# Kernel tuning notes

Measured on AMD Instinct MI355X. Metric: run time of the kernel, lower is better.

## Reference

```python
import jax, jax.numpy as jnp
import numpy as np

N_NODES = 50000
N_RAND_EDGES = 800000
IN_DIM = 128
HEADS = 4
OUT_FEATS = 32
NEG_SLOPE = 0.2  # DGL GATConv default


def setup_inputs() -> dict:
    key = jax.random.key(0)
    k1, k2, k3, k4, k5, k6 = jax.random.split(key, 6)
    h = jax.random.normal(k1, (N_NODES, IN_DIM), dtype=jnp.float32)
    fc_w = jax.random.normal(k2, (HEADS * OUT_FEATS, IN_DIM), dtype=jnp.float32) * 0.1
    attn_l = jax.random.normal(k3, (HEADS, OUT_FEATS), dtype=jnp.float32) * 0.1
    attn_r = jax.random.normal(k4, (HEADS, OUT_FEATS), dtype=jnp.float32) * 0.1
    src_r = jax.random.randint(k5, (N_RAND_EDGES,), 0, N_NODES, dtype=jnp.int32)
    dst_r = jax.random.randint(k6, (N_RAND_EDGES,), 0, N_NODES, dtype=jnp.int32)
    loops = jnp.arange(N_NODES, dtype=jnp.int32)
    src = jnp.concatenate([src_r, loops])  # self-loops ensure in_degree >= 1
    dst = jnp.concatenate([dst_r, loops])
    return {"h": h, "fc_w": fc_w, "attn_l": attn_l, "attn_r": attn_r,
            "src": src, "dst": dst}


def reference(h, fc_w, attn_l, attn_r, src, dst):
    N = h.shape[0]
    # linear projection, reshape to [N, H, D]
    hf = (h @ fc_w.T).reshape(N, HEADS, OUT_FEATS)
    # per-node attention halves: el = <hf, a_l>, er = <hf, a_r>  -> [N, H]
    el = jnp.einsum('nhd,hd->nh', hf, attn_l)
    er = jnp.einsum('nhd,hd->nh', hf, attn_r)
    # edge scores: u_add_v + leaky_relu  -> [E, H]
    e = jax.nn.leaky_relu(el[src] + er[dst], negative_slope=NEG_SLOPE)
    # segment softmax over incoming edges of each dst node
    m = jax.ops.segment_max(e, dst, num_segments=N)
    ex = jnp.exp(e - m[dst])
    s = jax.ops.segment_sum(ex, dst, num_segments=N)
    a = ex / s[dst]  # [E, H]
    # weighted neighbor aggregation: u_mul_e then segment sum
    msg = hf[src] * a[:, :, None]  # [E, H, D]
    out = jax.ops.segment_sum(msg, dst, num_segments=N)  # [N, H, D]
    return out.reshape(N, HEADS * OUT_FEATS), a[:, :, None]
```

## Files before the change

### kernel.cpp

```cpp
#include <hip/hip_runtime.h>
#include <hip/hip_bf16.h>

#define NEG 0.2f
#define BSTRIDE 8192

typedef float vf4 __attribute__((ext_vector_type(4)));
typedef int   vi4 __attribute__((ext_vector_type(4)));
typedef short bf8 __attribute__((ext_vector_type(8)));
typedef float f32x4 __attribute__((ext_vector_type(4)));

__device__ __forceinline__ float leaky(float x){ return x > 0.f ? x : NEG*x; }
__device__ __forceinline__ float sel4(float4 q, int head){
  float lo = (head & 1) ? q.y : q.x;
  float hi = (head & 1) ? q.w : q.z;
  return (head & 2) ? hi : lo;
}
__device__ __forceinline__ float b2f_lo(unsigned u){ return __uint_as_float(u << 16); }
__device__ __forceinline__ float b2f_hi(unsigned u){ return __uint_as_float(u & 0xffff0000u); }
__device__ __forceinline__ float b2f(unsigned short u){ return __uint_as_float((unsigned)u << 16); }
__device__ __forceinline__ unsigned short f2b(float f){
  __hip_bfloat16 b = __float2bfloat16(f);
  return *(unsigned short*)&b;
}
__device__ __forceinline__ vi4 ntload_i4(const int* p){
  return __builtin_nontemporal_load((const vi4*)p);
}
__device__ __forceinline__ void ntstore_f4(float* p, float a, float b, float c, float d){
  vf4 v; v.x = a; v.y = b; v.z = c; v.w = d;
  __builtin_nontemporal_store(v, (vf4*)p);
}

__global__ __launch_bounds__(256) void k_wconv(const float* __restrict__ fcw,
    unsigned short* __restrict__ fcw16, int* __restrict__ bcur) {
  const int tid = threadIdx.x;
  if (blockIdx.x == 0) bcur[tid] = tid * BSTRIDE;
  const int i = (blockIdx.x*256 + tid) * 8;
  float4 w0 = *(const float4*)&fcw[i];
  float4 w1 = *(const float4*)&fcw[i + 4];
  unsigned short q[8];
  q[0]=f2b(w0.x); q[1]=f2b(w0.y); q[2]=f2b(w0.z); q[3]=f2b(w0.w);
  q[4]=f2b(w1.x); q[5]=f2b(w1.y); q[6]=f2b(w1.z); q[7]=f2b(w1.w);
  *(uint4*)&fcw16[i] = *(const uint4*)q;
}

__global__ __launch_bounds__(256) void k_proj(
    const float* __restrict__ h, const unsigned short* __restrict__ fcw16,
    const float* __restrict__ attn_l, const float* __restrict__ attn_r,
    unsigned short* __restrict__ hf16, float* __restrict__ el, float* __restrict__ er, int N)
{
  __shared__ __align__(16) unsigned short hs[4][16*128];

  const int tid = threadIdx.x;
  const int wave = tid >> 6, lane = tid & 63;
  const int r = lane & 15, khi = lane >> 4;
  const int nb0 = blockIdx.x*64 + wave*16;
  int gn_a = nb0 + r; if (gn_a >= N) gn_a = N-1;
  const float* hp = &h[(size_t)gn_a*128];

  bf8 afr[4];
  #pragma unroll
  for (int ks = 0; ks < 4; ++ks) {
    const float* p = hp + ks*32 + khi*8;
    float4 w0 = *(const float4*)p;
    float4 w1 = *(const float4*)(p + 4);
    bf8 a;
    a[0]=(short)f2b(w0.x); a[1]=(short)f2b(w0.y); a[2]=(short)f2b(w0.z); a[3]=(short)f2b(w0.w);
    a[4]=(short)f2b(w1.x); a[5]=(short)f2b(w1.y); a[6]=(short)f2b(w1.z); a[7]=(short)f2b(w1.w);
    afr[ks] = a;
  }

  f32x4 acc[8];
  #pragma unroll
  for (int ct = 0; ct < 8; ++ct) { acc[ct][0]=0.f; acc[ct][1]=0.f; acc[ct][2]=0.f; acc[ct][3]=0.f; }

  #pragma unroll
  for (int ct = 0; ct < 8; ++ct) {
    const int f = ct*16 + r;
    #pragma unroll
    for (int ks = 0; ks < 4; ++ks) {
      bf8 b = *(const bf8*)&fcw16[(size_t)f*128 + ks*32 + khi*8];
      acc[ct] = __builtin_amdgcn_mfma_f32_16x16x32_bf16(afr[ks], b, acc[ct], 0, 0, 0);
    }
  }

  unsigned short* hw = &hs[wave][0];
  #pragma unroll
  for (int ct = 0; ct < 8; ++ct) {
    const int ftile = ct*16 + r;
    #pragma unroll
    for (int j = 0; j < 4; ++j)
      hw[(khi*4 + j)*128 + ftile] = f2b(acc[ct][j]);
  }

  for (int i = lane; i < 16*16; i += 64) {
    int row = i >> 4, ch = i & 15;
    int gn = nb0 + row;
    if (gn < N)
      *(uint4*)&hf16[(size_t)gn*128 + ch*8] = *(const uint4*)&hw[row*128 + ch*8];
  }

  {
    const int row = lane >> 2, head = lane & 3;
    const int gn = nb0 + row;
    const unsigned short* hr = &hw[row*128 + head*32];
    const float* alp = &attn_l[head*32];
    const float* arp = &attn_r[head*32];
    float e_l = 0.f, e_r = 0.f;
    #pragma unroll
    for (int ff = 0; ff < 32; ++ff) {
      float hv = b2f(hr[ff]);
      e_l += hv * alp[ff];
      e_r += hv * arp[ff];
    }
    if (gn < N) {
      el[(size_t)gn*4 + head] = e_l;
      er[(size_t)gn*4 + head] = e_r;
    }
  }
}

#define TILE 4096
__global__ __launch_bounds__(1024) void k_bin(
    const int* __restrict__ src, const int* __restrict__ dst,
    int* __restrict__ bcur, unsigned int* __restrict__ staging, int E)
{
  __shared__ unsigned int lpack[TILE];
  __shared__ unsigned char lbkt[TILE];
  __shared__ unsigned short sidx[TILE];
  __shared__ int lhist[256], lbase[256], lcur[256], gbase[256];

  const int t = threadIdx.x;
  const int e0 = blockIdx.x * TILE;
  const int cnt = min(TILE, E - e0);

  if (t < 256) lhist[t] = 0;
  __syncthreads();

  for (int i = t; i < cnt; i += 1024) {
    int s = __builtin_nontemporal_load(&src[e0 + i]);
    int d = __builtin_nontemporal_load(&dst[e0 + i]);
    lpack[i] = ((unsigned)(d & 255) << 24) | (unsigned)s;
    int b = d >> 8;
    lbkt[i] = (unsigned char)b;
    atomicAdd(&lhist[b], 1);
  }
  __syncthreads();

  __shared__ int ltmp[256];
  if (t < 256) ltmp[t] = lhist[t];
  __syncthreads();
  for (int off = 1; off < 256; off <<= 1) {
    int x = 0;
    if (t < 256 && t >= off) x = ltmp[t - off];
    __syncthreads();
    if (t < 256) ltmp[t] += x;
    __syncthreads();
  }
  if (t < 256) { lbase[t] = ltmp[t] - lhist[t]; lcur[t] = ltmp[t] - lhist[t]; }
  __syncthreads();

  for (int i = t; i < cnt; i += 1024) {
    int p = atomicAdd(&lcur[lbkt[i]], 1);
    sidx[p] = (unsigned short)i;
  }
  if (t < 256) {
    int c = lhist[t];
    gbase[t] = c ? atomicAdd(&bcur[t], c) : 0;
  }
  __syncthreads();

  for (int p = t; p < cnt; p += 1024) {
    int j = sidx[p];
    int b = lbkt[j];
    staging[gbase[b] + (p - lbase[b])] = lpack[j];
  }
}

__global__ __launch_bounds__(1024) void k_debin(
    const unsigned int* __restrict__ staging, const int* __restrict__ bcur,
    int* __restrict__ esrc, int* __restrict__ offsets, int* __restrict__ degs, int N)
{
  __shared__ int lout[BSTRIDE];
  __shared__ int lhist[256], lexcl[256], lcur[256];

  const int t = threadIdx.x;
  const int b = blockIdx.x;
  const int n0 = b << 8;
  const int nb = min(256, N - n0);
  const int out_start = b * BSTRIDE;
  const int cnt = bcur[b] - out_start;

  if (t < 256) lhist[t] = 0;
  __syncthreads();

  for (int i = t; i < cnt; i += 1024)
    atomicAdd(&lhist[staging[out_start + i] >> 24], 1);
  __syncthreads();

  if (t < 256) lexcl[t] = lhist[t];
  __syncthreads();
  for (int off = 1; off < 256; off <<= 1) {
    int x = 0;
    if (t < 256 && t >= off) x = lexcl[t - off];
    __syncthreads();
    if (t < 256) lexcl[t] += x;
    __syncthreads();
  }
  if (t < 256) {
    int ex = lexcl[t] - lhist[t];
    lexcl[t] = ex;
    lcur[t]  = ex;
  }
  __syncthreads();

  for (int i = t; i < cnt; i += 1024) {
    unsigned int w = staging[out_start + i];
    int p = atomicAdd(&lcur[w >> 24], 1);
    lout[p] = (int)(w & 0x00FFFFFFu);
  }
  __syncthreads();
  for (int i = t; i < cnt; i += 1024)
    esrc[out_start + i] = lout[i];

  if (t < nb) {
    offsets[n0 + t] = out_start + lexcl[t];
    degs[n0 + t]    = lhist[t];
  }
}

__global__ __launch_bounds__(256) void k_aggr(
    const int* __restrict__ esrc, const int* __restrict__ offsets, const int* __restrict__ degs,
    const unsigned short* __restrict__ hf16, const float* __restrict__ el, const float* __restrict__ er,
    float* __restrict__ out, float* __restrict__ mr, int N)
{
  __shared__ float as[4][64][4];
  __shared__ int   es[4][64];
  const int wave = threadIdx.x >> 6, lane = threadIdx.x & 63;
  const int v = blockIdx.x*4 + wave;
  if (v >= N) return;
  const int start = offsets[v];
  const int deg   = degs[v];
  const float4 er4 = *(const float4*)&er[(size_t)v*4];

  const bool act = lane < deg;
  float4 x4 = make_float4(0.f, 0.f, 0.f, 0.f);
  int mys = 0;
  if (act) {
    mys = esrc[start + lane];
    float4 el4 = *(const float4*)&el[(size_t)mys*4];
    x4.x = __expf(leaky(el4.x + er4.x));
    x4.y = __expf(leaky(el4.y + er4.y));
    x4.z = __expf(leaky(el4.z + er4.z));
    x4.w = __expf(leaky(el4.w + er4.w));
  }
  float4 s4 = x4;
  for (int j = lane + 64; j < deg; j += 64) {
    int s = esrc[start + j];
    float4 el4 = *(const float4*)&el[(size_t)s*4];
    s4.x += __expf(leaky(el4.x + er4.x));
    s4.y += __expf(leaky(el4.y + er4.y));
    s4.z += __expf(leaky(el4.z + er4.z));
    s4.w += __expf(leaky(el4.w + er4.w));
  }
  #pragma unroll
  for (int mm = 32; mm; mm >>= 1) {
    s4.x += __shfl_xor(s4.x, mm);
    s4.y += __shfl_xor(s4.y, mm);
    s4.z += __shfl_xor(s4.z, mm);
    s4.w += __shfl_xor(s4.w, mm);
  }
  const float4 r4 = make_float4(1.f/s4.x, 1.f/s4.y, 1.f/s4.z, 1.f/s4.w);

  if (act) {
    float4 a4 = make_float4(x4.x*r4.x, x4.y*r4.y, x4.z*r4.z, x4.w*r4.w);
    *(float4*)&as[wave][lane][0] = a4;
    es[wave][lane] = mys;
  }
  if (lane == 0) *(float4*)&mr[(size_t)v*4] = r4;

  const int g = lane >> 3;
  const int l = lane & 7;
  const int head = l >> 1;
  float acc[16];
  #pragma unroll
  for (int k = 0; k < 16; ++k) acc[k] = 0.f;

  const int degL = deg < 64 ? deg : 64;
  {
    int je = g;
    int jec = je < degL ? je : 0;
    int sj = es[wave][jec];
    float a = je < degL ? as[wave][jec][head] : 0.f;
    const unsigned short* hp = &hf16[(size_t)sj*128 + 16*l];
    uint4 q0 = *(const uint4*)hp;
    uint4 q1 = *(const uint4*)(hp + 8);
    for (int j = 0; j < degL; j += 8) {
      int je2 = j + 8 + g;
      int jec2 = je2 < degL ? je2 : 0;
      int s2 = es[wave][jec2];
      float a2 = je2 < degL ? as[wave][jec2][head] : 0.f;
      const unsigned short* hp2 = &hf16[(size_t)s2*128 + 16*l];
      uint4 p0 = *(const uint4*)hp2;
      uint4 p1 = *(const uint4*)(hp2 + 8);
      acc[0]  += a*b2f_lo(q0.x); acc[1]  += a*b2f_hi(q0.x);
      acc[2]  += a*b2f_lo(q0.y); acc[3]  += a*b2f_hi(q0.y);
      acc[4]  += a*b2f_lo(q0.z); acc[5]  += a*b2f_hi(q0.z);
      acc[6]  += a*b2f_lo(q0.w); acc[7]  += a*b2f_hi(q0.w);
      acc[8]  += a*b2f_lo(q1.x); acc[9]  += a*b2f_hi(q1.x);
      acc[10] += a*b2f_lo(q1.y); acc[11] += a*b2f_hi(q1.y);
      acc[12] += a*b2f_lo(q1.z); acc[13] += a*b2f_hi(q1.z);
      acc[14] += a*b2f_lo(q1.w); acc[15] += a*b2f_hi(q1.w);
      q0 = p0; q1 = p1; a = a2;
    }
  }
  for (int j = 64; j < deg; j += 8) {
    const int je = j + g;
    const bool valid = je < deg;
    int s = esrc[start + (valid ? je : 0)];
    float rh = sel4(r4, head), erh = sel4(er4, head);
    float a = __expf(leaky(el[(size_t)s*4 + head] + erh)) * rh;
    if (!valid) a = 0.f;
    const unsigned short* hp = &hf16[(size_t)s*128 + 16*l];
    uint4 q0 = *(const uint4*)hp;
    uint4 q1 = *(const uint4*)(hp + 8);
    acc[0]  += a*b2f_lo(q0.x); acc[1]  += a*b2f_hi(q0.x);
    acc[2]  += a*b2f_lo(q0.y); acc[3]  += a*b2f_hi(q0.y);
    acc[4]  += a*b2f_lo(q0.z); acc[5]  += a*b2f_hi(q0.z);
    acc[6]  += a*b2f_lo(q0.w); acc[7]  += a*b2f_hi(q0.w);
    acc[8]  += a*b2f_lo(q1.x); acc[9]  += a*b2f_hi(q1.x);
    acc[10] += a*b2f_lo(q1.y); acc[11] += a*b2f_hi(q1.y);
    acc[12] += a*b2f_lo(q1.z); acc[13] += a*b2f_hi(q1.z);
    acc[14] += a*b2f_lo(q1.w); acc[15] += a*b2f_hi(q1.w);
  }

  #pragma unroll
  for (int k = 0; k < 16; ++k) {
    acc[k] += __shfl_xor(acc[k], 8);
    acc[k] += __shfl_xor(acc[k], 16);
    acc[k] += __shfl_xor(acc[k], 32);
  }
  if (g == 0) {
    float* op = &out[(size_t)v*128 + 16*l];
    ntstore_f4(op,      acc[0],  acc[1],  acc[2],  acc[3]);
    ntstore_f4(op + 4,  acc[4],  acc[5],  acc[6],  acc[7]);
    ntstore_f4(op + 8,  acc[8],  acc[9],  acc[10], acc[11]);
    ntstore_f4(op + 12, acc[12], acc[13], acc[14], acc[15]);
  }
}

__global__ void k_attn(const int* __restrict__ src, const int* __restrict__ dst,
                       const float* __restrict__ el, const float* __restrict__ er,
                       const float* __restrict__ mr, float* __restrict__ a_out, int E) {
  int e0 = (blockIdx.x*256 + threadIdx.x)*4;
  if (e0 + 3 < E) {
    vi4 sv = ntload_i4(&src[e0]);
    vi4 dv = ntload_i4(&dst[e0]);
    #pragma unroll
    for (int k = 0; k < 4; ++k) {
      int s = (k==0)?sv.x:(k==1)?sv.y:(k==2)?sv.z:sv.w;
      int d = (k==0)?dv.x:(k==1)?dv.y:(k==2)?dv.z:dv.w;
      float4 el4 = *(const float4*)&el[(size_t)s*4];
      float4 er4 = *(const float4*)&er[(size_t)d*4];
      float4 c4  = *(const float4*)&mr[(size_t)d*4];
      ntstore_f4(&a_out[(size_t)(e0+k)*4],
                 __expf(leaky(el4.x + er4.x)) * c4.x,
                 __expf(leaky(el4.y + er4.y)) * c4.y,
                 __expf(leaky(el4.z + er4.z)) * c4.z,
                 __expf(leaky(el4.w + er4.w)) * c4.w);
    }
  } else {
    for (int e = e0; e < E; ++e) {
      int s = src[e], d = dst[e];
      float4 el4 = *(const float4*)&el[(size_t)s*4];
      float4 er4 = *(const float4*)&er[(size_t)d*4];
      float4 c4  = *(const float4*)&mr[(size_t)d*4];
      ntstore_f4(&a_out[(size_t)e*4],
                 __expf(leaky(el4.x + er4.x)) * c4.x,
                 __expf(leaky(el4.y + er4.y)) * c4.y,
                 __expf(leaky(el4.z + er4.z)) * c4.z,
                 __expf(leaky(el4.w + er4.w)) * c4.w);
    }
  }
}

extern "C" void kernel_launch(void* const* d_in, const int* in_sizes, int n_in,
                              void* d_out, int out_size, void* d_ws, size_t ws_size,
                              hipStream_t stream) {
  const float* h      = (const float*)d_in[0];
  const float* fcw    = (const float*)d_in[1];
  const float* attn_l = (const float*)d_in[2];
  const float* attn_r = (const float*)d_in[3];
  const int*   src    = (const int*)d_in[4];
  const int*   dst    = (const int*)d_in[5];
  const int N = in_sizes[0] / 128;
  const int E = in_sizes[4];
  const int B = (N + 255) >> 8;

  float* out   = (float*)d_out;
  float* a_out = out + (size_t)N*128;

  char* w = (char*)d_ws;
  unsigned short* hf16 = (unsigned short*)w; w += (size_t)N*128*sizeof(unsigned short);
  unsigned short* fcw16 = (unsigned short*)w; w += (size_t)128*128*sizeof(unsigned short);
  float* el      = (float*)w; w += (size_t)N*4*sizeof(float);
  float* er      = (float*)w; w += (size_t)N*4*sizeof(float);
  float* mr      = (float*)w; w += (size_t)N*4*sizeof(float);
  int*   esrc    = (int*)w;   w += (size_t)256*BSTRIDE*sizeof(int);
  unsigned int* staging = (unsigned int*)w; w += (size_t)256*BSTRIDE*sizeof(unsigned int);
  int*   offsets = (int*)w;   w += (size_t)N*sizeof(int);
  int*   degs    = (int*)w;   w += (size_t)N*sizeof(int);
  int*   bcur    = (int*)w;   w += 256*sizeof(int);

  k_wconv<<<8, 256, 0, stream>>>(fcw, fcw16, bcur);

  k_proj<<<(N + 63)/64, 256, 0, stream>>>(h, fcw16, attn_l, attn_r, hf16, el, er, N);

  k_bin<<<(E + TILE - 1)/TILE, 1024, 0, stream>>>(src, dst, bcur, staging, E);
  k_debin<<<B, 1024, 0, stream>>>(staging, bcur, esrc, offsets, degs, N);

  k_aggr<<<(N + 3)/4, 256, 0, stream>>>(esrc, offsets, degs, hf16, el, er, out, mr, N);

  k_attn<<<(E/4 + 255)/256 + 1, 256, 0, stream>>>(src, dst, el, er, mr, a_out, E);
}
```

Baseline: 116.3 us.

## Fuse weight bf16 conversion into projection kernel with swizzled LDS weight tile

Removes the separate weight-conversion kernel. Each projection block now converts the fp32 weight matrix to bf16 into a 32KB XOR-swizzled LDS tile and reads MFMA B fragments from LDS rather than global memory. Each block now handles 128 nodes in two passes, which amortises the per-block conversion. This saves one kernel launch and the global re-reads of the weights, but every block redoes the conversion and the larger LDS footprint reduces occupancy.

```diff
diff --git a/kernel.cpp b/kernel.cpp
--- a/kernel.cpp
+++ b/kernel.cpp
@@ -30,91 +30,97 @@
   __builtin_nontemporal_store(v, (vf4*)p);
 }
 
-__global__ __launch_bounds__(256) void k_wconv(const float* __restrict__ fcw,
-    unsigned short* __restrict__ fcw16, int* __restrict__ bcur) {
+__global__ __launch_bounds__(256) void k_proj(
+    const float* __restrict__ h, const float* __restrict__ fcw,
+    const float* __restrict__ attn_l, const float* __restrict__ attn_r,
+    unsigned short* __restrict__ hf16, float* __restrict__ el, float* __restrict__ er,
+    int* __restrict__ bcur, int N)
+{
+  __shared__ __align__(16) unsigned short fcs[128*128];
+  __shared__ __align__(16) unsigned short hs[4][16*128];
+
   const int tid = threadIdx.x;
   if (blockIdx.x == 0) bcur[tid] = tid * BSTRIDE;
-  const int i = (blockIdx.x*256 + tid) * 8;
-  float4 w0 = *(const float4*)&fcw[i];
-  float4 w1 = *(const float4*)&fcw[i + 4];
-  unsigned short q[8];
-  q[0]=f2b(w0.x); q[1]=f2b(w0.y); q[2]=f2b(w0.z); q[3]=f2b(w0.w);
-  q[4]=f2b(w1.x); q[5]=f2b(w1.y); q[6]=f2b(w1.z); q[7]=f2b(w1.w);
-  *(uint4*)&fcw16[i] = *(const uint4*)q;
-}
-
-__global__ __launch_bounds__(256) void k_proj(
-    const float* __restrict__ h, const unsigned short* __restrict__ fcw16,
-    const float* __restrict__ attn_l, const float* __restrict__ attn_r,
-    unsigned short* __restrict__ hf16, float* __restrict__ el, float* __restrict__ er, int N)
-{
-  __shared__ __align__(16) unsigned short hs[4][16*128];
-
-  const int tid = threadIdx.x;
+
+  for (int i = tid; i < 128*16; i += 256) {
+    int f = i >> 4, ch = i & 15;
+    const float* p = &fcw[(size_t)f*128 + ch*8];
+    float4 w0 = *(const float4*)p;
+    float4 w1 = *(const float4*)(p + 4);
+    unsigned short* q = &fcs[f*128 + (ch ^ (f & 7))*8];
+    q[0]=f2b(w0.x); q[1]=f2b(w0.y); q[2]=f2b(w0.z); q[3]=f2b(w0.w);
+    q[4]=f2b(w1.x); q[5]=f2b(w1.y); q[6]=f2b(w1.z); q[7]=f2b(w1.w);
+  }
+  __syncthreads();
+
   const int wave = tid >> 6, lane = tid & 63;
   const int r = lane & 15, khi = lane >> 4;
-  const int nb0 = blockIdx.x*64 + wave*16;
-  int gn_a = nb0 + r; if (gn_a >= N) gn_a = N-1;
-  const float* hp = &h[(size_t)gn_a*128];
-
-  bf8 afr[4];
-  #pragma unroll
-  for (int ks = 0; ks < 4; ++ks) {
-    const float* p = hp + ks*32 + khi*8;
-    float4 w0 = *(const float4*)p;
-    float4 w1 = *(const float4*)(p + 4);
-    bf8 a;
-    a[0]=(short)f2b(w0.x); a[1]=(short)f2b(w0.y); a[2]=(short)f2b(w0.z); a[3]=(short)f2b(w0.w);
-    a[4]=(short)f2b(w1.x); a[5]=(short)f2b(w1.y); a[6]=(short)f2b(w1.z); a[7]=(short)f2b(w1.w);
-    afr[ks] = a;
-  }
-
-  f32x4 acc[8];
-  #pragma unroll
-  for (int ct = 0; ct < 8; ++ct) { acc[ct][0]=0.f; acc[ct][1]=0.f; acc[ct][2]=0.f; acc[ct][3]=0.f; }
-
-  #pragma unroll
-  for (int ct = 0; ct < 8; ++ct) {
-    const int f = ct*16 + r;
+
+  for (int nt = 0; nt < 2; ++nt) {
+    const int nb0 = blockIdx.x*128 + nt*64 + wave*16;
+    int gn_a = nb0 + r; if (gn_a >= N) gn_a = N-1;
+    const float* hp = &h[(size_t)gn_a*128];
+
+    bf8 afr[4];
     #pragma unroll
     for (int ks = 0; ks < 4; ++ks) {
-      bf8 b = *(const bf8*)&fcw16[(size_t)f*128 + ks*32 + khi*8];
-      acc[ct] = __builtin_amdgcn_mfma_f32_16x16x32_bf16(afr[ks], b, acc[ct], 0, 0, 0);
-    }
-  }
-
-  unsigned short* hw = &hs[wave][0];
-  #pragma unroll
-  for (int ct = 0; ct < 8; ++ct) {
-    const int ftile = ct*16 + r;
+      const float* p = hp + ks*32 + khi*8;
+      float4 w0 = *(const float4*)p;
+      float4 w1 = *(const float4*)(p + 4);
+      bf8 a;
+      a[0]=(short)f2b(w0.x); a[1]=(short)f2b(w0.y); a[2]=(short)f2b(w0.z); a[3]=(short)f2b(w0.w);
+      a[4]=(short)f2b(w1.x); a[5]=(short)f2b(w1.y); a[6]=(short)f2b(w1.z); a[7]=(short)f2b(w1.w);
+      afr[ks] = a;
+    }
+
+    f32x4 acc[8];
     #pragma unroll
-    for (int j = 0; j < 4; ++j)
-      hw[(khi*4 + j)*128 + ftile] = f2b(acc[ct][j]);
-  }
-
-  for (int i = lane; i < 16*16; i += 64) {
-    int row = i >> 4, ch = i & 15;
-    int gn = nb0 + row;
-    if (gn < N)
-      *(uint4*)&hf16[(size_t)gn*128 + ch*8] = *(const uint4*)&hw[row*128 + ch*8];
-  }
-
-  {
-    const int row = lane >> 2, head = lane & 3;
-    const int gn = nb0 + row;
-    const unsigned short* hr = &hw[row*128 + head*32];
-    const float* alp = &attn_l[head*32];
-    const float* arp = &attn_r[head*32];
-    float e_l = 0.f, e_r = 0.f;
+    for (int ct = 0; ct < 8; ++ct) { acc[ct][0]=0.f; acc[ct][1]=0.f; acc[ct][2]=0.f; acc[ct][3]=0.f; }
+
     #pragma unroll
-    for (int ff = 0; ff < 32; ++ff) {
-      float hv = b2f(hr[ff]);
-      e_l += hv * alp[ff];
-      e_r += hv * arp[ff];
-    }
-    if (gn < N) {
-      el[(size_t)gn*4 + head] = e_l;
-      er[(size_t)gn*4 + head] = e_r;
+    for (int ct = 0; ct < 8; ++ct) {
+      const int f = ct*16 + r;
+      #pragma unroll
+      for (int ks = 0; ks < 4; ++ks) {
+        const int ch = (ks*4 + khi) ^ (f & 7);
+        bf8 b = *(const bf8*)&fcs[f*128 + ch*8];
+        acc[ct] = __builtin_amdgcn_mfma_f32_16x16x32_bf16(afr[ks], b, acc[ct], 0, 0, 0);
+      }
+    }
+
+    unsigned short* hw = &hs[wave][0];
+    #pragma unroll
+    for (int ct = 0; ct < 8; ++ct) {
+      const int ftile = ct*16 + r;
+      #pragma unroll
+      for (int j = 0; j < 4; ++j)
+        hw[(khi*4 + j)*128 + ftile] = f2b(acc[ct][j]);
+    }
+
+    for (int i = lane; i < 16*16; i += 64) {
+      int row = i >> 4, ch = i & 15;
+      int gn = nb0 + row;
+      if (gn < N)
+        *(uint4*)&hf16[(size_t)gn*128 + ch*8] = *(const uint4*)&hw[row*128 + ch*8];
+    }
+
+    {
+      const int row = lane >> 2, head = lane & 3;
+      const int gn = nb0 + row;
+      const unsigned short* hr = &hw[row*128 + head*32];
+      const float* alp = &attn_l[head*32];
+      const float* arp = &attn_r[head*32];
+      float e_l = 0.f, e_r = 0.f;
+      #pragma unroll
+      for (int ff = 0; ff < 32; ++ff) {
+        float hv = b2f(hr[ff]);
+        e_l += hv * alp[ff];
+        e_r += hv * arp[ff];
+      }
+      if (gn < N) {
+        el[(size_t)gn*4 + head] = e_l;
+        er[(size_t)gn*4 + head] = e_r;
+      }
     }
   }
 }
@@ -401,7 +407,6 @@
 
   char* w = (char*)d_ws;
   unsigned short* hf16 = (unsigned short*)w; w += (size_t)N*128*sizeof(unsigned short);
-  unsigned short* fcw16 = (unsigned short*)w; w += (size_t)128*128*sizeof(unsigned short);
   float* el      = (float*)w; w += (size_t)N*4*sizeof(float);
   float* er      = (float*)w; w += (size_t)N*4*sizeof(float);
   float* mr      = (float*)w; w += (size_t)N*4*sizeof(float);
@@ -411,9 +416,7 @@
   int*   degs    = (int*)w;   w += (size_t)N*sizeof(int);
   int*   bcur    = (int*)w;   w += 256*sizeof(int);
 
-  k_wconv<<<8, 256, 0, stream>>>(fcw, fcw16, bcur);
-
-  k_proj<<<(N + 63)/64, 256, 0, stream>>>(h, fcw16, attn_l, attn_r, hf16, el, er, N);
+  k_proj<<<(N + 127)/128, 256, 0, stream>>>(h, fcw, attn_l, attn_r, hf16, el, er, bcur, N);
 
   k_bin<<<(E + TILE - 1)/TILE, 1024, 0, stream>>>(src, dst, bcur, staging, E);
   k_debin<<<B, 1024, 0, stream>>>(staging, bcur, esrc, offsets, degs, N);
```

New measurement: 107.0 us. 8.0% less time.
